# Performance work log

Measured on AMD Instinct MI355X. Metric: run time of the kernel, lower is better.

Reference implementation:

```python
import jax, jax.numpy as jnp
import numpy as np
from jax import lax

H = 64  # hidden size for all 4 layers

def _run_layer(inp, Wi, Wh, bi, bh):
    # inp: [B, T, D_in]; Wi: [H, D_in]; Wh: [H, H]; bi, bh: [H]
    # PyTorch RNN cell: h_t = tanh(x_t @ Wi^T + bi + h_{t-1} @ Wh^T + bh)
    pre = jnp.einsum('btd,hd->bth', inp, Wi) + (bi + bh)  # input part, batched GEMM
    B = inp.shape[0]
    h0 = jnp.zeros((B, H), dtype=inp.dtype)

    def step(h, x_t):
        h_new = jnp.tanh(x_t + h @ Wh.T)
        return h_new, h_new

    _, ys = lax.scan(step, h0, pre.transpose(1, 0, 2))  # scan over time
    return ys.transpose(1, 0, 2)  # [B, T, H]


def setup_inputs() -> dict:
    key = jax.random.key(0)
    ks = jax.random.split(key, 12)
    B, T, D_in = 512, 1024, 52
    s_in = 1.0 / np.sqrt(H)  # PyTorch RNN init scale U(-1/sqrt(H), 1/sqrt(H))
    u = lambda k, shape: jax.random.uniform(k, shape, jnp.float32, -s_in, s_in)
    return {
        'x': jax.random.normal(ks[0], (B, T, D_in), jnp.float32),
        'Wih0': u(ks[1], (H, D_in)),
        'Whh0': u(ks[2], (H, H)),
        'bih0': u(ks[3], (H,)),
        'bhh0': u(ks[4], (H,)),
        'Wih': u(ks[5], (3, H, H)),   # layers 1..3 input weights
        'Whh': u(ks[6], (3, H, H)),
        'bih': u(ks[7], (3, H)),
        'bhh': u(ks[8], (3, H)),
        'Wfc': u(ks[9], (64, H)),     # fc: Linear(64, output_dims=64)
        'bfc': u(ks[10], (64,)),
    }


def reference(x, Wih0, Whh0, bih0, bhh0, Wih, Whh, bih, bhh, Wfc, bfc):
    h = _run_layer(x, Wih0, Whh0, bih0, bhh0)
    for l in range(3):  # fixed small layer loop
        h = _run_layer(h, Wih[l], Whh[l], bih[l], bhh[l])
    y = jnp.einsum('bth,oh->bto', h, Wfc) + bfc
    return y
```

## Files before the change

kernel.cpp:

```cpp
#include <hip/hip_runtime.h>


typedef __fp16 h2 __attribute__((ext_vector_type(2)));

__device__ __forceinline__ h2 pk2(float a, float b) {
#if __has_builtin(__builtin_amdgcn_cvt_pkrtz)
  return __builtin_amdgcn_cvt_pkrtz(a, b);
#else
  h2 r; r.x = (__fp16)a; r.y = (__fp16)b; return r;
#endif
}

__device__ __forceinline__ float fdot2f(h2 a, h2 b, float c) {
#if __has_builtin(__builtin_amdgcn_fdot2)
  return __builtin_amdgcn_fdot2(a, b, c, false);
#else
  return c + (float)a.x * (float)b.x + (float)a.y * (float)b.y;
#endif
}

__device__ __forceinline__ h2 bc(unsigned int u) {
  return __builtin_bit_cast(h2, u);
}

__device__ __forceinline__ unsigned int ubc(h2 v) {
  return __builtin_bit_cast(unsigned int, v);
}

__device__ __forceinline__ float fast_tanh(float x) {
  float e = __expf(2.0f * x);
#if __has_builtin(__builtin_amdgcn_rcpf)
  return 1.0f - 2.0f * __builtin_amdgcn_rcpf(e + 1.0f);
#else
  return 1.0f - 2.0f / (e + 1.0f);
#endif
}

#define T_STEPS 1024

#define GEMV64(RES, HPTR, INIT)                               \
  do {                                                        \
    const uint4* hp_ = (const uint4*)(HPTR);                  \
    float a0_ = (INIT), a1_ = 0.f, a2_ = 0.f, a3_ = 0.f;      \
    _Pragma("unroll")                                         \
    for (int q_ = 0; q_ < 8; ++q_) {                          \
      uint4 u_ = hp_[q_];                                     \
      a0_ = fdot2f(bc(u_.x), w[4 * q_ + 0], a0_);             \
      a1_ = fdot2f(bc(u_.y), w[4 * q_ + 1], a1_);             \
      a2_ = fdot2f(bc(u_.z), w[4 * q_ + 2], a2_);             \
      a3_ = fdot2f(bc(u_.w), w[4 * q_ + 3], a3_);             \
    }                                                         \
    RES = (a0_ + a1_) + (a2_ + a3_);                          \
  } while (0)

#define PREGEMV(RES, XPTR)                                    \
  do {                                                        \
    const uint4* xp_ = (const uint4*)(XPTR);                  \
    float a0_ = bias0, a1_ = 0.f, a2_ = 0.f, a3_ = 0.f;       \
    _Pragma("unroll")                                         \
    for (int q_ = 0; q_ < 7; ++q_) {                          \
      uint4 u_ = xp_[q_];                                     \
      a0_ = fdot2f(bc(u_.x), w0[4 * q_ + 0], a0_);            \
      a1_ = fdot2f(bc(u_.y), w0[4 * q_ + 1], a1_);            \
      a2_ = fdot2f(bc(u_.z), w0[4 * q_ + 2], a2_);            \
      a3_ = fdot2f(bc(u_.w), w0[4 * q_ + 3], a3_);            \
    }                                                         \
    RES = (a0_ + a1_) + (a2_ + a3_);                          \
  } while (0)

__global__ __launch_bounds__(512, 4) void rnn_fused(
    const float* __restrict__ x, const float* __restrict__ Wih0,
    const float* __restrict__ bih0, const float* __restrict__ bhh0,
    const float* __restrict__ Whh0, const float* __restrict__ Wih,
    const float* __restrict__ Whh, const float* __restrict__ bih,
    const float* __restrict__ bhh, const float* __restrict__ Wfc,
    const float* __restrict__ bfc, float* __restrict__ out) {
  const int tid  = threadIdx.x;
  const int lane = tid & 63;
  const int wv   = __builtin_amdgcn_readfirstlane(tid >> 6);
  const int b    = blockIdx.x;

  __shared__ __attribute__((aligned(16))) __fp16 hbuf[4][2][4][64];
  __shared__ __attribute__((aligned(16))) float PB[4][2][4][64];
  __shared__ __attribute__((aligned(16))) unsigned int pxs[2][4][28];

  ((float*)hbuf)[tid]       = 0.f;
  ((float*)hbuf)[tid + 512] = 0.f;

  const float* W;
  float bias = 0.f;
  int role, L;
  if (wv == 7) {
    role = 2; L = 3; W = Wfc; bias = bfc[lane];
  } else if ((wv & 1) == 0) {
    role = 0; L = wv >> 1;
    W = (L == 0) ? Whh0 : (Whh + (L - 1) * 4096);
    if (L > 0) bias = bih[(L - 1) * 64 + lane] + bhh[(L - 1) * 64 + lane];
  } else {
    role = 1; L = (wv + 1) >> 1;
    W = Wih + (L - 1) * 4096;
  }

  h2 w[32];
  {
    const float2* wsrc = (const float2*)(W + lane * 64);
#pragma unroll
    for (int k = 0; k < 32; ++k) {
      float2 v = wsrc[k];
      w[k] = pk2(v.x, v.y);
    }
  }

  h2 w0[28];
  float bias0 = 0.f;
  float4 xr = {0.f, 0.f, 0.f, 0.f};
  const float4* xg = (const float4*)(x + (long)b * T_STEPS * 52);
  const int xrow = (lane / 13) & 3;
  const int xcol = lane % 13;
  const bool xact = (lane < 52);

  if (wv == 1) {
    const float2* w2 = (const float2*)(Wih0 + lane * 52);
#pragma unroll
    for (int k = 0; k < 26; ++k) {
      float2 v = w2[k];
      w0[k] = pk2(v.x, v.y);
    }
    w0[26] = pk2(0.f, 0.f);
    w0[27] = pk2(0.f, 0.f);
    bias0 = bih0[lane] + bhh0[lane];
    if (lane < 16) pxs[lane >> 3][(lane >> 1) & 3][26 + (lane & 1)] = 0u;
    float4 xa = {0.f, 0.f, 0.f, 0.f}, xb = {0.f, 0.f, 0.f, 0.f};
    if (xact) {
      xa = xg[0 * 52 + lane];
      xb = xg[1 * 52 + lane];
      xr = xg[2 * 52 + lane];
      pxs[0][xrow][2 * xcol]     = ubc(pk2(xa.x, xa.y));
      pxs[0][xrow][2 * xcol + 1] = ubc(pk2(xa.z, xa.w));
      pxs[1][xrow][2 * xcol]     = ubc(pk2(xb.x, xb.y));
      pxs[1][xrow][2 * xcol + 1] = ubc(pk2(xb.z, xb.w));
    }
  }
  __syncthreads();

  if (wv == 1) {
    float pv;
    PREGEMV(pv, pxs[0][0]); PB[0][1][0][lane] = pv;
    PREGEMV(pv, pxs[0][1]); PB[0][1][1][lane] = pv;
    PREGEMV(pv, pxs[0][2]); PB[0][1][2][lane] = pv;
    PREGEMV(pv, pxs[0][3]); PB[0][1][3][lane] = pv;
  }
  __syncthreads();

  float* op = out + (long)b * T_STEPS * 64 + lane;

#pragma unroll 1
  for (int k = 0; k < 256 + 7; ++k) {
    const unsigned kk = (unsigned)(k - wv);
    const int rd = (k - 1) & 1;
    const int wr = k & 1;
    if (kk < 256u) {
      if (role == 0) {
        float p0_ = PB[L][rd][0][lane];
        float p1_ = PB[L][rd][1][lane];
        float p2_ = PB[L][rd][2][lane];
        float p3_ = PB[L][rd][3][lane];
        float hv;
        GEMV64(hv, hbuf[L][rd][3], bias);
        float h0v = fast_tanh(hv + p0_);
        hbuf[L][wr][0][lane] = (__fp16)h0v;
        GEMV64(hv, hbuf[L][wr][0], bias);
        float h1v = fast_tanh(hv + p1_);
        hbuf[L][wr][1][lane] = (__fp16)h1v;
        GEMV64(hv, hbuf[L][wr][1], bias);
        float h2v = fast_tanh(hv + p2_);
        hbuf[L][wr][2][lane] = (__fp16)h2v;
        GEMV64(hv, hbuf[L][wr][2], bias);
        float h3v = fast_tanh(hv + p3_);
        hbuf[L][wr][3][lane] = (__fp16)h3v;
      } else if (role == 1) {
        float q0, q1, q2, q3;
        GEMV64(q0, hbuf[L - 1][rd][0], 0.f);
        GEMV64(q1, hbuf[L - 1][rd][1], 0.f);
        GEMV64(q2, hbuf[L - 1][rd][2], 0.f);
        GEMV64(q3, hbuf[L - 1][rd][3], 0.f);
        PB[L][wr][0][lane] = q0;
        PB[L][wr][1][lane] = q1;
        PB[L][wr][2][lane] = q2;
        PB[L][wr][3][lane] = q3;
      } else {
        float q0, q1, q2, q3;
        GEMV64(q0, hbuf[3][rd][0], bias);
        GEMV64(q1, hbuf[3][rd][1], bias);
        GEMV64(q2, hbuf[3][rd][2], bias);
        GEMV64(q3, hbuf[3][rd][3], bias);
        op[0]   = q0;
        op[64]  = q1;
        op[128] = q2;
        op[192] = q3;
        op += 256;
      }
    }
    if (wv == 1) {
      if (k <= 254) {
        const unsigned int* xsrc = &pxs[(k + 1) & 1][0][0];
        float pv;
        PREGEMV(pv, xsrc + 0 * 28); PB[0][wr][0][lane] = pv;
        PREGEMV(pv, xsrc + 1 * 28); PB[0][wr][1][lane] = pv;
        PREGEMV(pv, xsrc + 2 * 28); PB[0][wr][2][lane] = pv;
        PREGEMV(pv, xsrc + 3 * 28); PB[0][wr][3][lane] = pv;
      }
      if (k <= 253 && xact) {
        float4 xw = xr;
        if (k <= 252) xr = xg[(k + 3) * 52 + lane];
        pxs[k & 1][xrow][2 * xcol]     = ubc(pk2(xw.x, xw.y));
        pxs[k & 1][xrow][2 * xcol + 1] = ubc(pk2(xw.z, xw.w));
      }
    }
    __syncthreads();
  }
}

extern "C" void kernel_launch(void* const* d_in, const int* in_sizes, int n_in,
                              void* d_out, int out_size, void* d_ws,
                              size_t ws_size, hipStream_t stream) {
  const float* x    = (const float*)d_in[0];
  const float* Wih0 = (const float*)d_in[1];
  const float* Whh0 = (const float*)d_in[2];
  const float* bih0 = (const float*)d_in[3];
  const float* bhh0 = (const float*)d_in[4];
  const float* Wih  = (const float*)d_in[5];
  const float* Whh  = (const float*)d_in[6];
  const float* bih  = (const float*)d_in[7];
  const float* bhh  = (const float*)d_in[8];
  const float* Wfc  = (const float*)d_in[9];
  const float* bfc  = (const float*)d_in[10];
  float* out = (float*)d_out;

  const int B = in_sizes[0] / (T_STEPS * 52);
  (void)d_ws; (void)ws_size;

  rnn_fused<<<B, 512, 0, stream>>>(x, Wih0, bih0, bhh0, Whh0, Wih, Whh, bih,
                                   bhh, Wfc, bfc, out);
}
```

Measured before the change: 815.1 us.

## Split layer-0 input projection across two waves and move x loading to a third

The layer-0 input GEMV (52-wide) was done entirely by wave 1, which also loaded and packed x. It is now split into two 32-column halves computed by waves 1 and 3, with the second half written to a new PBb buffer that the layer-0 recurrence wave adds in. Wave 5 takes over the global x prefetch and packing. The aim is to shorten the per-step critical path of wave 1, which bounds each barrier interval. The cost is an extra shared buffer, padding of pxs to 32 words, and four extra LDS reads plus adds in the layer-0 recurrence wave.

```diff
diff --git a/kernel.cpp b/kernel.cpp
--- a/kernel.cpp
+++ b/kernel.cpp
@@ -53,12 +53,12 @@
     RES = (a0_ + a1_) + (a2_ + a3_);                          \
   } while (0)
 
-#define PREGEMV(RES, XPTR)                                    \
+#define PREGEMV16(RES, XPTR, INIT)                            \
   do {                                                        \
     const uint4* xp_ = (const uint4*)(XPTR);                  \
-    float a0_ = bias0, a1_ = 0.f, a2_ = 0.f, a3_ = 0.f;       \
+    float a0_ = (INIT), a1_ = 0.f, a2_ = 0.f, a3_ = 0.f;      \
     _Pragma("unroll")                                         \
-    for (int q_ = 0; q_ < 7; ++q_) {                          \
+    for (int q_ = 0; q_ < 4; ++q_) {                          \
       uint4 u_ = xp_[q_];                                     \
       a0_ = fdot2f(bc(u_.x), w0[4 * q_ + 0], a0_);            \
       a1_ = fdot2f(bc(u_.y), w0[4 * q_ + 1], a1_);            \
@@ -82,10 +82,12 @@
 
   __shared__ __attribute__((aligned(16))) __fp16 hbuf[4][2][4][64];
   __shared__ __attribute__((aligned(16))) float PB[4][2][4][64];
-  __shared__ __attribute__((aligned(16))) unsigned int pxs[2][4][28];
+  __shared__ __attribute__((aligned(16))) float PBb[2][4][64];
+  __shared__ __attribute__((aligned(16))) unsigned int pxs[2][4][32];
 
   ((float*)hbuf)[tid]       = 0.f;
   ((float*)hbuf)[tid + 512] = 0.f;
+  if (tid < 256) ((unsigned int*)pxs)[tid] = 0u;
 
   const float* W;
   float bias = 0.f;
@@ -111,7 +113,7 @@
     }
   }
 
-  h2 w0[28];
+  h2 w0[16];
   float bias0 = 0.f;
   float4 xr = {0.f, 0.f, 0.f, 0.f};
   const float4* xg = (const float4*)(x + (long)b * T_STEPS * 52);
@@ -119,21 +121,23 @@
   const int xcol = lane % 13;
   const bool xact = (lane < 52);
 
+  __syncthreads();
+
   if (wv == 1) {
     const float2* w2 = (const float2*)(Wih0 + lane * 52);
 #pragma unroll
-    for (int k = 0; k < 26; ++k) {
-      float2 v = w2[k];
-      w0[k] = pk2(v.x, v.y);
-    }
-    w0[26] = pk2(0.f, 0.f);
-    w0[27] = pk2(0.f, 0.f);
+    for (int q = 0; q < 16; ++q) { float2 v = w2[q]; w0[q] = pk2(v.x, v.y); }
     bias0 = bih0[lane] + bhh0[lane];
-    if (lane < 16) pxs[lane >> 3][(lane >> 1) & 3][26 + (lane & 1)] = 0u;
-    float4 xa = {0.f, 0.f, 0.f, 0.f}, xb = {0.f, 0.f, 0.f, 0.f};
+  } else if (wv == 3) {
+    const float2* w2 = (const float2*)(Wih0 + lane * 52);
+#pragma unroll
+    for (int q = 0; q < 10; ++q) { float2 v = w2[16 + q]; w0[q] = pk2(v.x, v.y); }
+#pragma unroll
+    for (int q = 10; q < 16; ++q) w0[q] = pk2(0.f, 0.f);
+  } else if (wv == 5) {
     if (xact) {
-      xa = xg[0 * 52 + lane];
-      xb = xg[1 * 52 + lane];
+      float4 xa = xg[0 * 52 + lane];
+      float4 xb = xg[1 * 52 + lane];
       xr = xg[2 * 52 + lane];
       pxs[0][xrow][2 * xcol]     = ubc(pk2(xa.x, xa.y));
       pxs[0][xrow][2 * xcol + 1] = ubc(pk2(xa.z, xa.w));
@@ -145,10 +149,16 @@
 
   if (wv == 1) {
     float pv;
-    PREGEMV(pv, pxs[0][0]); PB[0][1][0][lane] = pv;
-    PREGEMV(pv, pxs[0][1]); PB[0][1][1][lane] = pv;
-    PREGEMV(pv, pxs[0][2]); PB[0][1][2][lane] = pv;
-    PREGEMV(pv, pxs[0][3]); PB[0][1][3][lane] = pv;
+    PREGEMV16(pv, &pxs[0][0][0], bias0); PB[0][1][0][lane] = pv;
+    PREGEMV16(pv, &pxs[0][1][0], bias0); PB[0][1][1][lane] = pv;
+    PREGEMV16(pv, &pxs[0][2][0], bias0); PB[0][1][2][lane] = pv;
+    PREGEMV16(pv, &pxs[0][3][0], bias0); PB[0][1][3][lane] = pv;
+  } else if (wv == 3) {
+    float pv;
+    PREGEMV16(pv, &pxs[0][0][16], 0.f); PBb[1][0][lane] = pv;
+    PREGEMV16(pv, &pxs[0][1][16], 0.f); PBb[1][1][lane] = pv;
+    PREGEMV16(pv, &pxs[0][2][16], 0.f); PBb[1][2][lane] = pv;
+    PREGEMV16(pv, &pxs[0][3][16], 0.f); PBb[1][3][lane] = pv;
   }
   __syncthreads();
 
@@ -165,6 +175,12 @@
         float p1_ = PB[L][rd][1][lane];
         float p2_ = PB[L][rd][2][lane];
         float p3_ = PB[L][rd][3][lane];
+        if (L == 0) {
+          p0_ += PBb[rd][0][lane];
+          p1_ += PBb[rd][1][lane];
+          p2_ += PBb[rd][2][lane];
+          p3_ += PBb[rd][3][lane];
+        }
         float hv;
         GEMV64(hv, hbuf[L][rd][3], bias);
         float h0v = fast_tanh(hv + p0_);
@@ -205,11 +221,21 @@
       if (k <= 254) {
         const unsigned int* xsrc = &pxs[(k + 1) & 1][0][0];
         float pv;
-        PREGEMV(pv, xsrc + 0 * 28); PB[0][wr][0][lane] = pv;
-        PREGEMV(pv, xsrc + 1 * 28); PB[0][wr][1][lane] = pv;
-        PREGEMV(pv, xsrc + 2 * 28); PB[0][wr][2][lane] = pv;
-        PREGEMV(pv, xsrc + 3 * 28); PB[0][wr][3][lane] = pv;
-      }
+        PREGEMV16(pv, xsrc + 0 * 32, bias0); PB[0][wr][0][lane] = pv;
+        PREGEMV16(pv, xsrc + 1 * 32, bias0); PB[0][wr][1][lane] = pv;
+        PREGEMV16(pv, xsrc + 2 * 32, bias0); PB[0][wr][2][lane] = pv;
+        PREGEMV16(pv, xsrc + 3 * 32, bias0); PB[0][wr][3][lane] = pv;
+      }
+    } else if (wv == 3) {
+      if (k <= 254) {
+        const unsigned int* xsrc = &pxs[(k + 1) & 1][0][16];
+        float pv;
+        PREGEMV16(pv, xsrc + 0 * 32, 0.f); PBb[wr][0][lane] = pv;
+        PREGEMV16(pv, xsrc + 1 * 32, 0.f); PBb[wr][1][lane] = pv;
+        PREGEMV16(pv, xsrc + 2 * 32, 0.f); PBb[wr][2][lane] = pv;
+        PREGEMV16(pv, xsrc + 3 * 32, 0.f); PBb[wr][3][lane] = pv;
+      }
+    } else if (wv == 5) {
       if (k <= 253 && xact) {
         float4 xw = xr;
         if (k <= 252) xr = xg[(k + 3) * 52 + lane];
```

Result: faster. 708.8 us (-13.0%).

## Merge input projection into recurrent waves, shrinking block to five waves

Applied to the files above, without the earlier changes.

Each layer's input projection GEMV now runs in the same wave as its recurrent GEMV, so the separate projection waves and the PB shared buffer go away. The block drops from 8 to 5 waves, and the wavefront pipeline drains in 260 steps instead of 263. The fc wave now also loads x into shared memory. The per-step critical path in each layer wave grows by four extra GEMVs, in exchange for fewer waves, less LDS traffic and a shorter pipeline.

```diff
diff --git a/kernel.cpp b/kernel.cpp
--- a/kernel.cpp
+++ b/kernel.cpp
@@ -38,37 +38,37 @@
 
 #define T_STEPS 1024
 
-#define GEMV64(RES, HPTR, INIT)                               \
+#define GEMV64(RES, HPTR, WARR, INIT)                         \
   do {                                                        \
     const uint4* hp_ = (const uint4*)(HPTR);                  \
     float a0_ = (INIT), a1_ = 0.f, a2_ = 0.f, a3_ = 0.f;      \
     _Pragma("unroll")                                         \
     for (int q_ = 0; q_ < 8; ++q_) {                          \
       uint4 u_ = hp_[q_];                                     \
-      a0_ = fdot2f(bc(u_.x), w[4 * q_ + 0], a0_);             \
-      a1_ = fdot2f(bc(u_.y), w[4 * q_ + 1], a1_);             \
-      a2_ = fdot2f(bc(u_.z), w[4 * q_ + 2], a2_);             \
-      a3_ = fdot2f(bc(u_.w), w[4 * q_ + 3], a3_);             \
+      a0_ = fdot2f(bc(u_.x), WARR[4 * q_ + 0], a0_);          \
+      a1_ = fdot2f(bc(u_.y), WARR[4 * q_ + 1], a1_);          \
+      a2_ = fdot2f(bc(u_.z), WARR[4 * q_ + 2], a2_);          \
+      a3_ = fdot2f(bc(u_.w), WARR[4 * q_ + 3], a3_);          \
     }                                                         \
     RES = (a0_ + a1_) + (a2_ + a3_);                          \
   } while (0)
 
-#define PREGEMV(RES, XPTR)                                    \
+#define PREGEMV(RES, XPTR, INIT)                              \
   do {                                                        \
     const uint4* xp_ = (const uint4*)(XPTR);                  \
-    float a0_ = bias0, a1_ = 0.f, a2_ = 0.f, a3_ = 0.f;       \
+    float a0_ = (INIT), a1_ = 0.f, a2_ = 0.f, a3_ = 0.f;      \
     _Pragma("unroll")                                         \
     for (int q_ = 0; q_ < 7; ++q_) {                          \
       uint4 u_ = xp_[q_];                                     \
-      a0_ = fdot2f(bc(u_.x), w0[4 * q_ + 0], a0_);            \
-      a1_ = fdot2f(bc(u_.y), w0[4 * q_ + 1], a1_);            \
-      a2_ = fdot2f(bc(u_.z), w0[4 * q_ + 2], a2_);            \
-      a3_ = fdot2f(bc(u_.w), w0[4 * q_ + 3], a3_);            \
+      a0_ = fdot2f(bc(u_.x), wx_[4 * q_ + 0], a0_);           \
+      a1_ = fdot2f(bc(u_.y), wx_[4 * q_ + 1], a1_);           \
+      a2_ = fdot2f(bc(u_.z), wx_[4 * q_ + 2], a2_);           \
+      a3_ = fdot2f(bc(u_.w), wx_[4 * q_ + 3], a3_);           \
     }                                                         \
     RES = (a0_ + a1_) + (a2_ + a3_);                          \
   } while (0)
 
-__global__ __launch_bounds__(512, 4) void rnn_fused(
+__global__ __launch_bounds__(320, 4) void rnn_fused5(
     const float* __restrict__ x, const float* __restrict__ Wih0,
     const float* __restrict__ bih0, const float* __restrict__ bhh0,
     const float* __restrict__ Whh0, const float* __restrict__ Wih,
@@ -81,119 +81,105 @@
   const int b    = blockIdx.x;
 
   __shared__ __attribute__((aligned(16))) __fp16 hbuf[4][2][4][64];
-  __shared__ __attribute__((aligned(16))) float PB[4][2][4][64];
-  __shared__ __attribute__((aligned(16))) unsigned int pxs[2][4][28];
-
-  ((float*)hbuf)[tid]       = 0.f;
-  ((float*)hbuf)[tid + 512] = 0.f;
-
-  const float* W;
+  __shared__ __attribute__((aligned(16))) unsigned int pxs[2][4][32];
+
+  for (int i = tid; i < 1024; i += 320) ((unsigned int*)hbuf)[i] = 0u;
+  if (tid < 256) ((unsigned int*)pxs)[tid] = 0u;
+
+  const float* Wr;
   float bias = 0.f;
-  int role, L;
-  if (wv == 7) {
-    role = 2; L = 3; W = Wfc; bias = bfc[lane];
-  } else if ((wv & 1) == 0) {
-    role = 0; L = wv >> 1;
-    W = (L == 0) ? Whh0 : (Whh + (L - 1) * 4096);
-    if (L > 0) bias = bih[(L - 1) * 64 + lane] + bhh[(L - 1) * 64 + lane];
+  if (wv == 4) {
+    Wr = Wfc; bias = bfc[lane];
+  } else if (wv == 0) {
+    Wr = Whh0;
   } else {
-    role = 1; L = (wv + 1) >> 1;
-    W = Wih + (L - 1) * 4096;
-  }
-
-  h2 w[32];
+    Wr = Whh + (wv - 1) * 4096;
+    bias = bih[(wv - 1) * 64 + lane] + bhh[(wv - 1) * 64 + lane];
+  }
+
+  h2 wr_[32];
   {
-    const float2* wsrc = (const float2*)(W + lane * 64);
+    const float2* s = (const float2*)(Wr + lane * 64);
 #pragma unroll
-    for (int k = 0; k < 32; ++k) {
-      float2 v = wsrc[k];
-      w[k] = pk2(v.x, v.y);
-    }
-  }
-
-  h2 w0[28];
-  float bias0 = 0.f;
+    for (int q = 0; q < 32; ++q) { float2 v = s[q]; wr_[q] = pk2(v.x, v.y); }
+  }
+
+  h2 wx_[32];
+  float preb = 0.f;
+  if (wv == 0) {
+    const float2* s = (const float2*)(Wih0 + lane * 52);
+#pragma unroll
+    for (int q = 0; q < 26; ++q) { float2 v = s[q]; wx_[q] = pk2(v.x, v.y); }
+    wx_[26] = pk2(0.f, 0.f);
+    wx_[27] = pk2(0.f, 0.f);
+    preb = bih0[lane] + bhh0[lane];
+  } else if (wv <= 3) {
+    const float2* s = (const float2*)(Wih + (wv - 1) * 4096 + lane * 64);
+#pragma unroll
+    for (int q = 0; q < 32; ++q) { float2 v = s[q]; wx_[q] = pk2(v.x, v.y); }
+  }
+
   float4 xr = {0.f, 0.f, 0.f, 0.f};
   const float4* xg = (const float4*)(x + (long)b * T_STEPS * 52);
   const int xrow = (lane / 13) & 3;
   const int xcol = lane % 13;
   const bool xact = (lane < 52);
 
-  if (wv == 1) {
-    const float2* w2 = (const float2*)(Wih0 + lane * 52);
-#pragma unroll
-    for (int k = 0; k < 26; ++k) {
-      float2 v = w2[k];
-      w0[k] = pk2(v.x, v.y);
-    }
-    w0[26] = pk2(0.f, 0.f);
-    w0[27] = pk2(0.f, 0.f);
-    bias0 = bih0[lane] + bhh0[lane];
-    if (lane < 16) pxs[lane >> 3][(lane >> 1) & 3][26 + (lane & 1)] = 0u;
-    float4 xa = {0.f, 0.f, 0.f, 0.f}, xb = {0.f, 0.f, 0.f, 0.f};
-    if (xact) {
-      xa = xg[0 * 52 + lane];
-      xb = xg[1 * 52 + lane];
-      xr = xg[2 * 52 + lane];
-      pxs[0][xrow][2 * xcol]     = ubc(pk2(xa.x, xa.y));
-      pxs[0][xrow][2 * xcol + 1] = ubc(pk2(xa.z, xa.w));
-      pxs[1][xrow][2 * xcol]     = ubc(pk2(xb.x, xb.y));
-      pxs[1][xrow][2 * xcol + 1] = ubc(pk2(xb.z, xb.w));
-    }
-  }
   __syncthreads();
 
-  if (wv == 1) {
-    float pv;
-    PREGEMV(pv, pxs[0][0]); PB[0][1][0][lane] = pv;
-    PREGEMV(pv, pxs[0][1]); PB[0][1][1][lane] = pv;
-    PREGEMV(pv, pxs[0][2]); PB[0][1][2][lane] = pv;
-    PREGEMV(pv, pxs[0][3]); PB[0][1][3][lane] = pv;
+  if (wv == 4 && xact) {
+    float4 xa = xg[lane];
+    xr = xg[52 + lane];
+    pxs[0][xrow][2 * xcol]     = ubc(pk2(xa.x, xa.y));
+    pxs[0][xrow][2 * xcol + 1] = ubc(pk2(xa.z, xa.w));
   }
   __syncthreads();
 
   float* op = out + (long)b * T_STEPS * 64 + lane;
 
 #pragma unroll 1
-  for (int k = 0; k < 256 + 7; ++k) {
+  for (int k = 0; k < 256 + 4; ++k) {
     const unsigned kk = (unsigned)(k - wv);
-    const int rd = (k - 1) & 1;
-    const int wr = k & 1;
     if (kk < 256u) {
-      if (role == 0) {
-        float p0_ = PB[L][rd][0][lane];
-        float p1_ = PB[L][rd][1][lane];
-        float p2_ = PB[L][rd][2][lane];
-        float p3_ = PB[L][rd][3][lane];
+      const int rd = (int)((kk - 1) & 1u);
+      const int wr = (int)(kk & 1u);
+      if (wv == 0) {
+        float p0, p1, p2, p3;
+        PREGEMV(p0, &pxs[wr][0][0], preb);
+        PREGEMV(p1, &pxs[wr][1][0], preb);
+        PREGEMV(p2, &pxs[wr][2][0], preb);
+        PREGEMV(p3, &pxs[wr][3][0], preb);
         float hv;
-        GEMV64(hv, hbuf[L][rd][3], bias);
-        float h0v = fast_tanh(hv + p0_);
-        hbuf[L][wr][0][lane] = (__fp16)h0v;
-        GEMV64(hv, hbuf[L][wr][0], bias);
-        float h1v = fast_tanh(hv + p1_);
-        hbuf[L][wr][1][lane] = (__fp16)h1v;
-        GEMV64(hv, hbuf[L][wr][1], bias);
-        float h2v = fast_tanh(hv + p2_);
-        hbuf[L][wr][2][lane] = (__fp16)h2v;
-        GEMV64(hv, hbuf[L][wr][2], bias);
-        float h3v = fast_tanh(hv + p3_);
-        hbuf[L][wr][3][lane] = (__fp16)h3v;
-      } else if (role == 1) {
-        float q0, q1, q2, q3;
-        GEMV64(q0, hbuf[L - 1][rd][0], 0.f);
-        GEMV64(q1, hbuf[L - 1][rd][1], 0.f);
-        GEMV64(q2, hbuf[L - 1][rd][2], 0.f);
-        GEMV64(q3, hbuf[L - 1][rd][3], 0.f);
-        PB[L][wr][0][lane] = q0;
-        PB[L][wr][1][lane] = q1;
-        PB[L][wr][2][lane] = q2;
-        PB[L][wr][3][lane] = q3;
+        GEMV64(hv, hbuf[0][rd][3], wr_, 0.f);
+        float h0v = fast_tanh(hv + p0); hbuf[0][wr][0][lane] = (__fp16)h0v;
+        GEMV64(hv, hbuf[0][wr][0], wr_, 0.f);
+        float h1v = fast_tanh(hv + p1); hbuf[0][wr][1][lane] = (__fp16)h1v;
+        GEMV64(hv, hbuf[0][wr][1], wr_, 0.f);
+        float h2v = fast_tanh(hv + p2); hbuf[0][wr][2][lane] = (__fp16)h2v;
+        GEMV64(hv, hbuf[0][wr][2], wr_, 0.f);
+        float h3v = fast_tanh(hv + p3); hbuf[0][wr][3][lane] = (__fp16)h3v;
+      } else if (wv <= 3) {
+        const int L = wv;
+        float p0, p1, p2, p3;
+        GEMV64(p0, hbuf[L - 1][wr][0], wx_, 0.f);
+        GEMV64(p1, hbuf[L - 1][wr][1], wx_, 0.f);
+        GEMV64(p2, hbuf[L - 1][wr][2], wx_, 0.f);
+        GEMV64(p3, hbuf[L - 1][wr][3], wx_, 0.f);
+        float hv;
+        GEMV64(hv, hbuf[L][rd][3], wr_, bias);
+        float h0v = fast_tanh(hv + p0); hbuf[L][wr][0][lane] = (__fp16)h0v;
+        GEMV64(hv, hbuf[L][wr][0], wr_, bias);
+        float h1v = fast_tanh(hv + p1); hbuf[L][wr][1][lane] = (__fp16)h1v;
+        GEMV64(hv, hbuf[L][wr][1], wr_, bias);
+        float h2v = fast_tanh(hv + p2); hbuf[L][wr][2][lane] = (__fp16)h2v;
+        GEMV64(hv, hbuf[L][wr][2], wr_, bias);
+        float h3v = fast_tanh(hv + p3); hbuf[L][wr][3][lane] = (__fp16)h3v;
       } else {
         float q0, q1, q2, q3;
-        GEMV64(q0, hbuf[3][rd][0], bias);
-        GEMV64(q1, hbuf[3][rd][1], bias);
-        GEMV64(q2, hbuf[3][rd][2], bias);
-        GEMV64(q3, hbuf[3][rd][3], bias);
+        GEMV64(q0, hbuf[3][wr][0], wr_, bias);
+        GEMV64(q1, hbuf[3][wr][1], wr_, bias);
+        GEMV64(q2, hbuf[3][wr][2], wr_, bias);
+        GEMV64(q3, hbuf[3][wr][3], wr_, bias);
         op[0]   = q0;
         op[64]  = q1;
         op[128] = q2;
@@ -201,21 +187,11 @@
         op += 256;
       }
     }
-    if (wv == 1) {
-      if (k <= 254) {
-        const unsigned int* xsrc = &pxs[(k + 1) & 1][0][0];
-        float pv;
-        PREGEMV(pv, xsrc + 0 * 28); PB[0][wr][0][lane] = pv;
-        PREGEMV(pv, xsrc + 1 * 28); PB[0][wr][1][lane] = pv;
-        PREGEMV(pv, xsrc + 2 * 28); PB[0][wr][2][lane] = pv;
-        PREGEMV(pv, xsrc + 3 * 28); PB[0][wr][3][lane] = pv;
-      }
-      if (k <= 253 && xact) {
-        float4 xw = xr;
-        if (k <= 252) xr = xg[(k + 3) * 52 + lane];
-        pxs[k & 1][xrow][2 * xcol]     = ubc(pk2(xw.x, xw.y));
-        pxs[k & 1][xrow][2 * xcol + 1] = ubc(pk2(xw.z, xw.w));
-      }
+    if (wv == 4 && k <= 254 && xact) {
+      float4 xw = xr;
+      if (k <= 253) xr = xg[(k + 2) * 52 + lane];
+      pxs[(k + 1) & 1][xrow][2 * xcol]     = ubc(pk2(xw.x, xw.y));
+      pxs[(k + 1) & 1][xrow][2 * xcol + 1] = ubc(pk2(xw.z, xw.w));
     }
     __syncthreads();
   }
@@ -240,6 +216,6 @@
   const int B = in_sizes[0] / (T_STEPS * 52);
   (void)d_ws; (void)ws_size;
 
-  rnn_fused<<<B, 512, 0, stream>>>(x, Wih0, bih0, bhh0, Whh0, Wih, Whh, bih,
-                                   bhh, Wfc, bfc, out);
-}
+  rnn_fused5<<<B, 320, 0, stream>>>(x, Wih0, bih0, bhh0, Whh0, Wih, Whh, bih,
+                                    bhh, Wfc, bfc, out);
+}
```

Result: slower. 850.2 us (+4.3%).
